# Performance work log

Hardware: AMD Instinct MI355X
Metric: run time of the kernel (lower is better)

Reference implementation:

```python
import jax, jax.numpy as jnp
import numpy as np

B, N, E, H = 16, 768, 1024, 16  # batch == heads so mask[i] (head-indexed, as in the source) is valid
D = E // H
MASK_P = 0.1
NEG = jnp.float32(-1e16)


def setup_inputs() -> dict:
    key = jax.random.key(0)
    ks = jax.random.split(key, 8)
    query = jax.random.normal(ks[0], (B, N, E), jnp.float32)
    key_t = jax.random.normal(ks[1], (B, N, E), jnp.float32)
    value = jax.random.normal(ks[2], (B, N, E), jnp.float32)
    u = jax.random.uniform(ks[3], (B, N))
    mask = jnp.where(u < MASK_P, -jnp.inf, 0.0).astype(jnp.float32)
    # per-head Linear(head_dim, head_dim, bias=False) weights, stacked over heads: (H, out=D, in=D)
    Wq = jax.random.normal(ks[4], (H, D, D), jnp.float32) * (1.0 / np.sqrt(D))
    Wk = jax.random.normal(ks[5], (H, D, D), jnp.float32) * (1.0 / np.sqrt(D))
    Wv = jax.random.normal(ks[6], (H, D, D), jnp.float32) * (1.0 / np.sqrt(D))
    Wf = jax.random.normal(ks[7], (E, E), jnp.float32) * (1.0 / np.sqrt(E))
    return {"query": query, "key": key_t, "value": value, "mask": mask,
            "Wq": Wq, "Wk": Wk, "Wv": Wv, "Wf": Wf}


def reference(query, key, value, mask, Wq, Wk, Wv, Wf):
    b, n, e = query.shape
    h = Wq.shape[0]
    d = e // h
    q = query.reshape(b, n, h, d)
    k = key.reshape(b, n, h, d)
    v = value.reshape(b, n, h, d)
    # per-head nn.Linear: x @ W[i].T  (W: (H, out, in))
    qh = jnp.einsum('bnhd,hed->bnhe', q, Wq)
    kh = jnp.einsum('bnhd,hed->bnhe', k, Wk)
    vh = jnp.einsum('bnhd,hed->bnhe', v, Wv)
    # scaled QK^T: divide by embed_size**0.5 (NOT head_dim) as in the source
    scores = jnp.einsum('bqhd,bkhd->bhqk', qh, kh) / jnp.sqrt(jnp.float32(e))  # (B,H,N,N)
    # faithful quirk: mask row selected by HEAD index i -> same additive mask for all batches
    bad = jnp.isneginf(mask)[:h]                      # (H, N)
    add = jnp.where(bad[:, :, None] | bad[:, None, :], NEG, jnp.float32(0.0))  # (H,N,N): row/col blanked
    probs = jax.nn.softmax(scores + add[None], axis=-1)
    attn = jnp.einsum('bhqk,bkhd->bqhd', probs, vh)   # (B,N,H,D)
    out = attn.reshape(b, n, e) @ Wf.T
    return out
```

## Files before the change

kernel.cpp:

```cpp
#include <hip/hip_runtime.h>

#define B_ 16
#define N_ 768
#define E_ 1024
#define H_ 16
#define D_ 64

typedef __bf16 bf16x8 __attribute__((ext_vector_type(8)));
typedef float f32x4 __attribute__((ext_vector_type(4)));
typedef unsigned short ushort8 __attribute__((ext_vector_type(8)));
typedef unsigned short ushort4v __attribute__((ext_vector_type(4)));
typedef unsigned int uint2v __attribute__((ext_vector_type(2)));
typedef unsigned int uint4v __attribute__((ext_vector_type(4)));

__device__ __forceinline__ unsigned short f2bf(float x) {
  unsigned u = __builtin_bit_cast(unsigned, x);
  u += 0x7FFFu + ((u >> 16) & 1u);
  return (unsigned short)(u >> 16);
}

__device__ __forceinline__ unsigned cvtpk(float lo, float hi) {
  unsigned r;
  asm("v_cvt_pk_bf16_f32 %0, %1, %2" : "=v"(r) : "v"(lo), "v"(hi));
  return r;
}

__device__ __forceinline__ float fexp2(float x) {
  float r;
  asm("v_exp_f32 %0, %1" : "=v"(r) : "v"(x));
  return r;
}

__device__ __forceinline__ f32x4 mfma16(ushort8 a, ushort8 b, f32x4 c) {
  return __builtin_amdgcn_mfma_f32_16x16x32_bf16(
      __builtin_bit_cast(bf16x8, a), __builtin_bit_cast(bf16x8, b), c, 0, 0, 0);
}

__global__ __launch_bounds__(256, 2) void proj_kernel(
    const float* __restrict__ q, const float* __restrict__ k, const float* __restrict__ v,
    const float* __restrict__ Wq, const float* __restrict__ Wk, const float* __restrict__ Wv,
    const float* __restrict__ Wf, unsigned short* __restrict__ Qh,
    unsigned short* __restrict__ Kh, unsigned short* __restrict__ Vt,
    unsigned short* __restrict__ Wfb) {
  const int m = blockIdx.x / 768;
  const int rest = blockIdx.x - m * 768;
  const int ng = rest % 3;
  const int bh = rest / 3;
  const int b = bh >> 4, h = bh & 15;
  const int nt0 = ng * 4;
  const int tid = threadIdx.x;
  const int w = tid >> 6, l = tid & 63;
  const int l16 = l & 15, lg = l >> 4;

  __shared__ __align__(16) unsigned short Xs[64][72];
  __shared__ __align__(16) unsigned short Ws[64][72];
  __shared__ __align__(16) unsigned short Os[64][72];

  const float* xp = (m == 0) ? q : (m == 1) ? k : v;
  const float* wp = ((m == 0) ? Wq : (m == 1) ? Wk : Wv) + (size_t)h * 4096;
  unsigned short* op = (m == 0) ? Qh : Kh;

  const int row = tid >> 4;
  const int c4 = (tid & 15) * 4;

  float4 wt[4], xt[4];
#pragma unroll
  for (int i = 0; i < 4; ++i)
    wt[i] = *(const float4*)&wp[(i * 16 + row) * 64 + c4];
#pragma unroll
  for (int i = 0; i < 4; ++i)
    xt[i] = *(const float4*)&xp[((size_t)(b * N_ + nt0 * 64 + i * 16 + row)) * E_ + h * 64 + c4];

  float4 wfv;
  if (blockIdx.x < 1024)
    wfv = *(const float4*)&Wf[((size_t)blockIdx.x * 256 + tid) * 4];

#pragma unroll
  for (int i = 0; i < 4; ++i) {
    ushort4v s;
    s[0] = f2bf(wt[i].x); s[1] = f2bf(wt[i].y); s[2] = f2bf(wt[i].z); s[3] = f2bf(wt[i].w);
    *(ushort4v*)&Ws[i * 16 + row][c4] = s;
  }
  if (blockIdx.x < 1024) {
    ushort4v s;
    s[0] = f2bf(wfv.x); s[1] = f2bf(wfv.y); s[2] = f2bf(wfv.z); s[3] = f2bf(wfv.w);
    *(ushort4v*)&Wfb[((size_t)blockIdx.x * 256 + tid) * 4] = s;
  }

  for (int t = 0; t < 4; ++t) {
#pragma unroll
    for (int i = 0; i < 4; ++i) {
      ushort4v s;
      s[0] = f2bf(xt[i].x); s[1] = f2bf(xt[i].y); s[2] = f2bf(xt[i].z); s[3] = f2bf(xt[i].w);
      *(ushort4v*)&Xs[i * 16 + row][c4] = s;
    }
    __syncthreads();

    if (t < 3) {
#pragma unroll
      for (int i = 0; i < 4; ++i)
        xt[i] = *(const float4*)&xp[((size_t)(b * N_ + (nt0 + t + 1) * 64 + i * 16 + row)) * E_ +
                                    h * 64 + c4];
    }

    f32x4 acc[4] = {};
#pragma unroll
    for (int kc = 0; kc < 2; ++kc) {
      ushort8 a = *(const ushort8*)&Xs[w * 16 + l16][kc * 32 + lg * 8];
#pragma unroll
      for (int eg = 0; eg < 4; ++eg) {
        ushort8 bf = *(const ushort8*)&Ws[eg * 16 + l16][kc * 32 + lg * 8];
        acc[eg] = mfma16(a, bf, acc[eg]);
      }
    }

    if (m < 2) {
#pragma unroll
      for (int eg = 0; eg < 4; ++eg)
#pragma unroll
        for (int r = 0; r < 4; ++r)
          Os[w * 16 + lg * 4 + r][eg * 16 + l16] = f2bf(acc[eg][r]);
    } else {
#pragma unroll
      for (int eg = 0; eg < 4; ++eg) {
        uint2v pk;
        pk[0] = cvtpk(acc[eg][0], acc[eg][1]);
        pk[1] = cvtpk(acc[eg][2], acc[eg][3]);
        *(uint2v*)&Os[eg * 16 + l16][w * 16 + lg * 4] = pk;
      }
    }
    __syncthreads();

    if (m < 2) {
#pragma unroll
      for (int i = 0; i < 2; ++i) {
        int rw = i * 32 + (tid >> 3), c8 = (tid & 7) * 8;
        *(ushort8*)&op[((size_t)(b * H_ + h) * N_ + (nt0 + t) * 64 + rw) * 64 + c8] =
            *(const ushort8*)&Os[rw][c8];
      }
    } else {
#pragma unroll
      for (int i = 0; i < 2; ++i) {
        int rw = i * 32 + (tid >> 3), c8 = (tid & 7) * 8;
        *(ushort8*)&Vt[((size_t)bh * 64 + rw) * N_ + (nt0 + t) * 64 + c8] =
            *(const ushort8*)&Os[rw][c8];
      }
    }
  }
}

__global__ __launch_bounds__(256, 4) void attn_kernel(
    const unsigned short* __restrict__ Qh, const unsigned short* __restrict__ Kh,
    const unsigned short* __restrict__ Vt, const float* __restrict__ mask,
    unsigned short* __restrict__ attnO) {
  const int bid = blockIdx.x;
  const int logical = (bid & 7) * 192 + (bid >> 3);
  const int qt = logical % 6;
  const int bh = logical / 6;
  const int b = bh >> 4, h = bh & 15;
  const int tid = threadIdx.x;
  const int w = tid >> 6, l = tid & 63;
  const int l16 = l & 15, lg = l >> 4;

  __shared__ __align__(16) unsigned short Ks[64][72];
  __shared__ __align__(16) unsigned short Vs[64][72];
  __shared__ float addk[N_];

  const size_t baseK = (size_t)bh * N_ * 64;
  const size_t baseV = (size_t)bh * 64 * N_;
  const int qrow0 = qt * 128 + w * 32;
  const float C2 = 0.04508422f;

  for (int i = tid; i < N_; i += 256)
    addk[i] = (mask[h * N_ + i] < -1e30f) ? -1.0e20f : 0.0f;

  ushort8 bQ[2][2];
#pragma unroll
  for (int qs = 0; qs < 2; ++qs)
#pragma unroll
    for (int kc = 0; kc < 2; ++kc)
      bQ[qs][kc] = *(const ushort8*)&Qh[((size_t)bh * N_ + qrow0 + qs * 16 + l16) * 64 +
                                        kc * 32 + lg * 8];
  float bqf[2];
#pragma unroll
  for (int qs = 0; qs < 2; ++qs)
    bqf[qs] = (mask[h * N_ + qrow0 + qs * 16 + l16] < -1e30f) ? 1.f : 0.f;

  const int srow = tid >> 3;
  const int sc8 = (tid & 7) * 8;

  uint4v kreg[2], vreg[2];
#pragma unroll
  for (int i = 0; i < 2; ++i) {
    int row = i * 32 + srow;
    kreg[i] = *(const uint4v*)&Kh[baseK + (size_t)row * 64 + sc8];
    vreg[i] = *(const uint4v*)&Vt[baseV + (size_t)row * N_ + sc8];
  }
  __syncthreads();
#pragma unroll
  for (int i = 0; i < 2; ++i) {
    int row = i * 32 + srow;
    *(ushort8*)&Ks[row][sc8] = __builtin_bit_cast(ushort8, kreg[i]);
    *(ushort8*)&Vs[row][sc8] = __builtin_bit_cast(ushort8, vreg[i]);
  }
  __syncthreads();

  f32x4 oacc[2][4] = {};
  float l_part[2] = {0.f, 0.f};

  for (int kt = 0; kt < 12; ++kt) {
    if (kt < 11) {
#pragma unroll
      for (int i = 0; i < 2; ++i) {
        int row = i * 32 + srow;
        kreg[i] = *(const uint4v*)&Kh[baseK + (size_t)((kt + 1) * 64 + row) * 64 + sc8];
        vreg[i] = *(const uint4v*)&Vt[baseV + (size_t)row * N_ + (kt + 1) * 64 + sc8];
      }
    }

    f32x4 st[4][2] = {};
#pragma unroll
    for (int kc = 0; kc < 2; ++kc) {
#pragma unroll
      for (int cg = 0; cg < 4; ++cg) {
        ushort8 aK = *(const ushort8*)&Ks[cg * 16 + l16][kc * 32 + lg * 8];
        st[cg][0] = mfma16(aK, bQ[0][kc], st[cg][0]);
        st[cg][1] = mfma16(aK, bQ[1][kc], st[cg][1]);
      }
    }

#pragma unroll
    for (int cg = 0; cg < 4; ++cg) {
      f32x4 ak4 = *(const f32x4*)&addk[kt * 64 + cg * 16 + lg * 4];
#pragma unroll
      for (int qs = 0; qs < 2; ++qs) {
#pragma unroll
        for (int r = 0; r < 4; ++r) {
          float t = __builtin_fmaf(st[cg][qs][r], C2, ak4[r]);
          t = (bqf[qs] > 0.f) ? 0.0f : t;
          float p = fexp2(t);
          l_part[qs] += p;
          st[cg][qs][r] = p;
        }
      }
    }

#pragma unroll
    for (int kcP = 0; kcP < 2; ++kcP) {
      ushort8 pa[2];
#pragma unroll
      for (int qs = 0; qs < 2; ++qs) {
        unsigned a0 = cvtpk(st[2 * kcP][qs][0], st[2 * kcP][qs][1]);
        unsigned b0 = cvtpk(st[2 * kcP][qs][2], st[2 * kcP][qs][3]);
        unsigned a1 = cvtpk(st[2 * kcP + 1][qs][0], st[2 * kcP + 1][qs][1]);
        unsigned b1 = cvtpk(st[2 * kcP + 1][qs][2], st[2 * kcP + 1][qs][3]);
        asm("v_permlane32_swap_b32 %0, %1" : "+v"(a0), "+v"(a1));
        asm("v_permlane16_swap_b32 %0, %1" : "+v"(a0), "+v"(a1));
        asm("v_permlane32_swap_b32 %0, %1" : "+v"(b0), "+v"(b1));
        asm("v_permlane16_swap_b32 %0, %1" : "+v"(b0), "+v"(b1));
        uint4v pk;
        pk[0] = a0; pk[1] = b0; pk[2] = a1; pk[3] = b1;
        pa[qs] = __builtin_bit_cast(ushort8, pk);
      }
#pragma unroll
      for (int dg = 0; dg < 4; ++dg) {
        ushort8 bv = *(const ushort8*)&Vs[dg * 16 + l16][kcP * 32 + lg * 8];
        oacc[0][dg] = mfma16(pa[0], bv, oacc[0][dg]);
        oacc[1][dg] = mfma16(pa[1], bv, oacc[1][dg]);
      }
    }

    __syncthreads();
    if (kt < 11) {
#pragma unroll
      for (int i = 0; i < 2; ++i) {
        int row = i * 32 + srow;
        *(ushort8*)&Ks[row][sc8] = __builtin_bit_cast(ushort8, kreg[i]);
        *(ushort8*)&Vs[row][sc8] = __builtin_bit_cast(ushort8, vreg[i]);
      }
    }
    __syncthreads();
  }

#pragma unroll
  for (int qs = 0; qs < 2; ++qs) {
    float s = l_part[qs];
    s += __shfl_xor(s, 16);
    s += __shfl_xor(s, 32);
#pragma unroll
    for (int r = 0; r < 4; ++r) {
      float dnm = __shfl(s, lg * 4 + r);
      float inv = 1.f / dnm;
      int qg = qrow0 + qs * 16 + lg * 4 + r;
      size_t orow = ((size_t)b * N_ + qg) * E_ + h * 64;
#pragma unroll
      for (int dg = 0; dg < 4; ++dg)
        attnO[orow + dg * 16 + l16] = f2bf(oacc[qs][dg][r] * inv);
    }
  }
}

__global__ __launch_bounds__(256) void gemm_kernel(const unsigned short* __restrict__ A,
                                                   const unsigned short* __restrict__ Bm,
                                                   float* __restrict__ out) {
  const int be = blockIdx.x & 7;
  const int bm = blockIdx.x >> 3;
  const int tid = threadIdx.x;
  const int w = tid >> 6, l = tid & 63;
  const int l16 = l & 15, lg = l >> 4;
  const int wm = w >> 1, wn = w & 1;

  __shared__ __align__(16) unsigned short As[128][72];
  __shared__ __align__(16) unsigned short Bs[128][72];

  f32x4 acc[4][4] = {};
  const int m0 = bm * 128, e0 = be * 128;
  const int srow = tid >> 3, sc8 = (tid & 7) * 8;
  const unsigned short* Ab = A + (size_t)(m0 + srow) * E_ + sc8;
  const unsigned short* Bb = Bm + (size_t)(e0 + srow) * E_ + sc8;

  uint4v ar[4], br[4];
#pragma unroll
  for (int i = 0; i < 4; ++i) {
    ar[i] = *(const uint4v*)(Ab + (size_t)i * 32 * E_);
    br[i] = *(const uint4v*)(Bb + (size_t)i * 32 * E_);
  }

  for (int kk = 0; kk < 16; ++kk) {
    __syncthreads();
#pragma unroll
    for (int i = 0; i < 4; ++i) {
      *(ushort8*)&As[i * 32 + srow][sc8] = __builtin_bit_cast(ushort8, ar[i]);
      *(ushort8*)&Bs[i * 32 + srow][sc8] = __builtin_bit_cast(ushort8, br[i]);
    }
    __syncthreads();
    if (kk < 15) {
#pragma unroll
      for (int i = 0; i < 4; ++i) {
        ar[i] = *(const uint4v*)(Ab + (size_t)i * 32 * E_ + (kk + 1) * 64);
        br[i] = *(const uint4v*)(Bb + (size_t)i * 32 * E_ + (kk + 1) * 64);
      }
    }
#pragma unroll
    for (int kc = 0; kc < 2; ++kc) {
      ushort8 a[4], bf[4];
#pragma unroll
      for (int i = 0; i < 4; ++i)
        a[i] = *(const ushort8*)&As[wm * 64 + i * 16 + l16][kc * 32 + lg * 8];
#pragma unroll
      for (int j = 0; j < 4; ++j)
        bf[j] = *(const ushort8*)&Bs[wn * 64 + j * 16 + l16][kc * 32 + lg * 8];
#pragma unroll
      for (int i = 0; i < 4; ++i)
#pragma unroll
        for (int j = 0; j < 4; ++j) acc[i][j] = mfma16(a[i], bf[j], acc[i][j]);
    }
  }

#pragma unroll
  for (int i = 0; i < 4; ++i)
#pragma unroll
    for (int j = 0; j < 4; ++j)
#pragma unroll
      for (int r = 0; r < 4; ++r)
        out[(size_t)(m0 + wm * 64 + i * 16 + lg * 4 + r) * E_ + e0 + wn * 64 + j * 16 + l16] =
            acc[i][j][r];
}

extern "C" void kernel_launch(void* const* d_in, const int* in_sizes, int n_in,
                              void* d_out, int out_size, void* d_ws, size_t ws_size,
                              hipStream_t stream) {
  const float* q = (const float*)d_in[0];
  const float* k = (const float*)d_in[1];
  const float* v = (const float*)d_in[2];
  const float* mask = (const float*)d_in[3];
  const float* Wq = (const float*)d_in[4];
  const float* Wk = (const float*)d_in[5];
  const float* Wv = (const float*)d_in[6];
  const float* Wf = (const float*)d_in[7];
  float* out = (float*)d_out;

  const size_t PH = (size_t)B_ * H_ * N_ * D_;
  unsigned short* Qh = (unsigned short*)d_ws;
  unsigned short* Kh = Qh + PH;
  unsigned short* Vt = Kh + PH;
  unsigned short* attn = Vt + PH;
  unsigned short* Wfb = attn + PH;

  proj_kernel<<<3 * B_ * H_ * (N_ / 256), 256, 0, stream>>>(q, k, v, Wq, Wk, Wv, Wf, Qh, Kh,
                                                            Vt, Wfb);
  attn_kernel<<<B_ * H_ * (N_ / 128), 256, 0, stream>>>(Qh, Kh, Vt, mask, attn);
  gemm_kernel<<<(B_ * N_ / 128) * (E_ / 128), 256, 0, stream>>>(attn, Wfb, out);
}
```

Baseline: 135.6 us.

## Drop LDS staging in projection kernel, use register MFMA fragments directly

The Q/K/V projection kernel no longer stages inputs, weights and outputs through shared memory. Each lane now loads its MFMA operand fragments straight from global memory, converts them with packed bf16 conversions, and writes results directly to global. This removes LDS traffic and both __syncthreads per tile. In exchange it drops the software prefetch of the next tile, and the Q/K outputs become scattered 2-byte stores rather than coalesced 16-byte ones.

```diff
diff --git a/kernel.cpp b/kernel.cpp
--- a/kernel.cpp
+++ b/kernel.cpp
@@ -34,6 +34,15 @@
 __device__ __forceinline__ f32x4 mfma16(ushort8 a, ushort8 b, f32x4 c) {
   return __builtin_amdgcn_mfma_f32_16x16x32_bf16(
       __builtin_bit_cast(bf16x8, a), __builtin_bit_cast(bf16x8, b), c, 0, 0, 0);
+}
+
+__device__ __forceinline__ ushort8 pack8(float4 u, float4 v) {
+  uint4v pk;
+  pk[0] = cvtpk(u.x, u.y);
+  pk[1] = cvtpk(u.z, u.w);
+  pk[2] = cvtpk(v.x, v.y);
+  pk[3] = cvtpk(v.z, v.w);
+  return __builtin_bit_cast(ushort8, pk);
 }
 
 __global__ __launch_bounds__(256, 2) void proj_kernel(
@@ -47,103 +56,65 @@
   const int ng = rest % 3;
   const int bh = rest / 3;
   const int b = bh >> 4, h = bh & 15;
-  const int nt0 = ng * 4;
   const int tid = threadIdx.x;
   const int w = tid >> 6, l = tid & 63;
   const int l16 = l & 15, lg = l >> 4;
 
-  __shared__ __align__(16) unsigned short Xs[64][72];
-  __shared__ __align__(16) unsigned short Ws[64][72];
-  __shared__ __align__(16) unsigned short Os[64][72];
-
   const float* xp = (m == 0) ? q : (m == 1) ? k : v;
   const float* wp = ((m == 0) ? Wq : (m == 1) ? Wk : Wv) + (size_t)h * 4096;
   unsigned short* op = (m == 0) ? Qh : Kh;
 
-  const int row = tid >> 4;
-  const int c4 = (tid & 15) * 4;
-
-  float4 wt[4], xt[4];
-#pragma unroll
-  for (int i = 0; i < 4; ++i)
-    wt[i] = *(const float4*)&wp[(i * 16 + row) * 64 + c4];
-#pragma unroll
-  for (int i = 0; i < 4; ++i)
-    xt[i] = *(const float4*)&xp[((size_t)(b * N_ + nt0 * 64 + i * 16 + row)) * E_ + h * 64 + c4];
-
-  float4 wfv;
-  if (blockIdx.x < 1024)
-    wfv = *(const float4*)&Wf[((size_t)blockIdx.x * 256 + tid) * 4];
-
-#pragma unroll
-  for (int i = 0; i < 4; ++i) {
-    ushort4v s;
-    s[0] = f2bf(wt[i].x); s[1] = f2bf(wt[i].y); s[2] = f2bf(wt[i].z); s[3] = f2bf(wt[i].w);
-    *(ushort4v*)&Ws[i * 16 + row][c4] = s;
-  }
   if (blockIdx.x < 1024) {
+    float4 wfv = *(const float4*)&Wf[((size_t)blockIdx.x * 256 + tid) * 4];
     ushort4v s;
     s[0] = f2bf(wfv.x); s[1] = f2bf(wfv.y); s[2] = f2bf(wfv.z); s[3] = f2bf(wfv.w);
     *(ushort4v*)&Wfb[((size_t)blockIdx.x * 256 + tid) * 4] = s;
   }
 
+  ushort8 bw[4][2];
+#pragma unroll
+  for (int eg = 0; eg < 4; ++eg)
+#pragma unroll
+    for (int kc = 0; kc < 2; ++kc) {
+      const float* wb = wp + (eg * 16 + l16) * 64 + kc * 32 + lg * 8;
+      bw[eg][kc] = pack8(*(const float4*)wb, *(const float4*)(wb + 4));
+    }
+
+  const int bn0base = ng * 256 + w * 16;
+  float4 xa[2][2][2];
+
+#pragma unroll 1
   for (int t = 0; t < 4; ++t) {
-#pragma unroll
-    for (int i = 0; i < 4; ++i) {
-      ushort4v s;
-      s[0] = f2bf(xt[i].x); s[1] = f2bf(xt[i].y); s[2] = f2bf(xt[i].z); s[3] = f2bf(xt[i].w);
-      *(ushort4v*)&Xs[i * 16 + row][c4] = s;
-    }
-    __syncthreads();
-
-    if (t < 3) {
-#pragma unroll
-      for (int i = 0; i < 4; ++i)
-        xt[i] = *(const float4*)&xp[((size_t)(b * N_ + (nt0 + t + 1) * 64 + i * 16 + row)) * E_ +
-                                    h * 64 + c4];
+    const size_t rowbase = ((size_t)(b * N_ + bn0base + t * 64 + l16)) * E_ + h * 64;
+#pragma unroll
+    for (int kc = 0; kc < 2; ++kc) {
+      const float* xb = xp + rowbase + kc * 32 + lg * 8;
+      xa[0][kc][0] = *(const float4*)xb;
+      xa[0][kc][1] = *(const float4*)(xb + 4);
     }
 
     f32x4 acc[4] = {};
 #pragma unroll
     for (int kc = 0; kc < 2; ++kc) {
-      ushort8 a = *(const ushort8*)&Xs[w * 16 + l16][kc * 32 + lg * 8];
-#pragma unroll
-      for (int eg = 0; eg < 4; ++eg) {
-        ushort8 bf = *(const ushort8*)&Ws[eg * 16 + l16][kc * 32 + lg * 8];
-        acc[eg] = mfma16(a, bf, acc[eg]);
-      }
-    }
-
+      ushort8 a = pack8(xa[0][kc][0], xa[0][kc][1]);
+#pragma unroll
+      for (int eg = 0; eg < 4; ++eg) acc[eg] = mfma16(a, bw[eg][kc], acc[eg]);
+    }
+
+    const int bn0 = bn0base + t * 64;
     if (m < 2) {
 #pragma unroll
       for (int eg = 0; eg < 4; ++eg)
 #pragma unroll
         for (int r = 0; r < 4; ++r)
-          Os[w * 16 + lg * 4 + r][eg * 16 + l16] = f2bf(acc[eg][r]);
+          op[((size_t)bh * N_ + bn0 + lg * 4 + r) * 64 + eg * 16 + l16] = f2bf(acc[eg][r]);
     } else {
 #pragma unroll
       for (int eg = 0; eg < 4; ++eg) {
         uint2v pk;
         pk[0] = cvtpk(acc[eg][0], acc[eg][1]);
         pk[1] = cvtpk(acc[eg][2], acc[eg][3]);
-        *(uint2v*)&Os[eg * 16 + l16][w * 16 + lg * 4] = pk;
-      }
-    }
-    __syncthreads();
-
-    if (m < 2) {
-#pragma unroll
-      for (int i = 0; i < 2; ++i) {
-        int rw = i * 32 + (tid >> 3), c8 = (tid & 7) * 8;
-        *(ushort8*)&op[((size_t)(b * H_ + h) * N_ + (nt0 + t) * 64 + rw) * 64 + c8] =
-            *(const ushort8*)&Os[rw][c8];
-      }
-    } else {
-#pragma unroll
-      for (int i = 0; i < 2; ++i) {
-        int rw = i * 32 + (tid >> 3), c8 = (tid & 7) * 8;
-        *(ushort8*)&Vt[((size_t)bh * 64 + rw) * N_ + (nt0 + t) * 64 + c8] =
-            *(const ushort8*)&Os[rw][c8];
+        *(uint2v*)&Vt[((size_t)bh * 64 + eg * 16 + l16) * N_ + bn0 + lg * 4] = pk;
       }
     }
   }
```

Measured after the change: 157.5 us. 16.1% more time.
